# Kernel tuning notes

Measured on AMD Instinct MI355X. Metric: run time of the kernel, lower is better.

## Reference

```python
import jax, jax.numpy as jnp
import numpy as np

B, H_HIST, S_DIM, HID, G, K, A = 1024, 16384, 32, 64, 10, 4, 8


def setup_inputs() -> dict:
    key = jax.random.key(0)
    ks = jax.random.split(key, 12)
    inp = {
        'state_batch': jax.random.normal(ks[0], (B, S_DIM), jnp.float32),
        'state_history_batch': jax.random.normal(ks[1], (H_HIST, S_DIM), jnp.float32),
        'joint_action_history_batch': jax.random.normal(ks[2], (H_HIST, G, A), jnp.float32),
        # per-abstract-agent encoder MLP: Linear(S->H) + ReLU, Linear(H->H) + ReLU, Linear(H->H) + ReLU
        'W0': jax.random.normal(ks[3], (K, S_DIM, HID), jnp.float32) / np.sqrt(S_DIM),
        'b0': jax.random.normal(ks[4], (K, HID), jnp.float32) * 0.01,
        'W1': jax.random.normal(ks[5], (K, HID, HID), jnp.float32) / np.sqrt(HID),
        'b1': jax.random.normal(ks[6], (K, HID), jnp.float32) * 0.01,
        'W2': jax.random.normal(ks[7], (K, HID, HID), jnp.float32) / np.sqrt(HID),
        'b2': jax.random.normal(ks[8], (K, HID), jnp.float32) * 0.01,
        'assignment_matrix': jnp.ones((G, K), jnp.float32),
    }
    return inp


def _encode(x, W0, b0, W1, b1, W2, b2):
    # x: [N, S_DIM] shared across K encoders -> [K, N, HID]
    h = jax.nn.relu(jnp.einsum('ni,kio->kno', x, W0) + b0[:, None, :])
    h = jax.nn.relu(jnp.einsum('kni,kio->kno', h, W1) + b1[:, None, :])
    h = jax.nn.relu(jnp.einsum('kni,kio->kno', h, W2) + b2[:, None, :])
    return h


def reference(state_batch, state_history_batch, joint_action_history_batch,
              W0, b0, W1, b1, W2, b2, assignment_matrix):
    enc_s = _encode(state_batch, W0, b0, W1, b1, W2, b2)            # [K, B, HID]
    enc_h = _encode(state_history_batch, W0, b0, W1, b1, W2, b2)    # [K, H, HID]
    # per (abstract agent k, batch item b): softmax over history of <enc_h, enc_s>
    attn = jax.nn.softmax(jnp.einsum('khd,kbd->kbh', enc_h, enc_s), axis=-1)  # [K, B, H]
    # weighted action aggregation: [H,G,A] contracted over H
    abs_pred = jnp.einsum('kbh,hga->kbga', attn, joint_action_history_batch)  # [K, B, G, A]
    soft_assign = jax.nn.softmax(assignment_matrix, axis=-1)                  # [G, K]
    out = jnp.einsum('gk,kbga->bga', soft_assign, abs_pred)                   # [B, G, A]
    return out
```

## Files before the change

kernel.cpp:

```cpp
#include <hip/hip_runtime.h>
#include <stdint.h>

#define B_SZ 1024
#define H_SZ 16384
#define SD   32
#define HID  64
#define G_SZ 10
#define K_SZ 4
#define A_SZ 8
#define VA   80

typedef float f32x4  __attribute__((ext_vector_type(4)));
typedef short bf16x8 __attribute__((ext_vector_type(8)));

__device__ inline short f2bf(float a) {
    unsigned u = __float_as_uint(a);
    return (short)((u + 0x7FFFu + ((u >> 16) & 1u)) >> 16);
}
__device__ inline void split_bf(float v, short& hi, short& lo) {
    hi = f2bf(v);
    lo = f2bf(v - __uint_as_float(((unsigned)(unsigned short)hi) << 16));
}
__device__ inline int cvt_pk_bf16(float a, float b) {
    int r;
    asm("v_cvt_pk_bf16_f32 %0, %1, %2" : "=v"(r) : "v"(a), "v"(b));
    return r;
}
__device__ inline void split2(float f0, float f1, int& hi, int& lo) {
    hi = cvt_pk_bf16(f0, f1);
    float r0 = f0 - __uint_as_float((unsigned)hi << 16);
    float r1 = f1 - __uint_as_float((unsigned)hi & 0xFFFF0000u);
    lo = cvt_pk_bf16(r0, r1);
}

__global__ __launch_bounds__(256) void k_prep(
    const float* __restrict__ W0, const float* __restrict__ W1,
    const float* __restrict__ W2,
    short* __restrict__ w0h, short* __restrict__ w0l,
    short* __restrict__ w1h, short* __restrict__ w1l,
    short* __restrict__ w2h, short* __restrict__ w2l)
{
    int idx = blockIdx.x * 256 + threadIdx.x;
    short hh, ll;
    if (idx < 8192) {
        int k = idx >> 11, r = idx & 2047;
        int i = r >> 6, jj = r & 63;
        int tt = jj >> 4, l15 = jj & 15;
        int quad = (i >> 3) & 3, e = i & 7;
        split_bf(W0[k * 2048 + i * 64 + jj], hh, ll);
        int dst = k * 2048 + tt * 512 + (quad * 16 + l15) * 8 + e;
        w0h[dst] = hh; w0l[dst] = ll;
    } else if (idx < 24576) {
        int d = idx - 8192;
        int k = d >> 12, r = d & 4095;
        int i = r >> 6, jj = r & 63;
        int kb = i >> 5, quad = (i >> 3) & 3, e = i & 7;
        int tt = jj >> 4, l15 = jj & 15;
        split_bf(W1[k * 4096 + i * 64 + jj], hh, ll);
        int dst = k * 4096 + tt * 1024 + kb * 512 + (quad * 16 + l15) * 8 + e;
        w1h[dst] = hh; w1l[dst] = ll;
    } else if (idx < 40960) {
        int d = idx - 24576;
        int k = d >> 12, r = d & 4095;
        int i = r >> 6, jj = r & 63;
        int kb = i >> 5, quad = (i >> 3) & 3, e = i & 7;
        int tt = jj >> 4, l15 = jj & 15;
        split_bf(W2[k * 4096 + i * 64 + jj], hh, ll);
        int dst = k * 4096 + tt * 1024 + kb * 512 + (quad * 16 + l15) * 8 + e;
        w2h[dst] = hh; w2l[dst] = ll;
    }
}

__global__ __launch_bounds__(256, 3) void k_encode(
    const float* __restrict__ state, const float* __restrict__ hist,
    const float* __restrict__ act,
    const short* __restrict__ w0fh, const short* __restrict__ w0fl,
    const short* __restrict__ w1fh, const short* __restrict__ w1fl,
    const short* __restrict__ w2fh, const short* __restrict__ w2fl,
    const float* __restrict__ b0, const float* __restrict__ b1,
    const float* __restrict__ b2,
    short* __restrict__ enc_s_h, short* __restrict__ enc_s_l,
    short* __restrict__ kf_h, short* __restrict__ kf_l,
    short* __restrict__ vf_h, short* __restrict__ vf_l)
{
    __shared__ __align__(16) short smem[18432];
    const int bid = blockIdx.x;
    const int t = threadIdx.x;

    if (bid >= 1088) {
        short* tile_h = smem;
        short* tile_l = smem + 5376;
        const int h0 = (bid - 1088) * 64;
        #pragma unroll
        for (int i = 0; i < 10; ++i) {
            int idx2 = 2 * (t + i * 256);
            float2 v = *(const float2*)(act + (size_t)h0 * VA + idx2);
            int h = idx2 / 80, c = idx2 - h * 80;
            int hi, lo; split2(v.x, v.y, hi, lo);
            *(int*)(tile_h + h * 84 + c) = hi;
            *(int*)(tile_l + h * 84 + c) = lo;
        }
        __syncthreads();
        #pragma unroll
        for (int i = 0; i < 3; ++i) {
            int jj = t + i * 256;
            if (jj < 640) {
                int va = jj >> 3, hb = jj & 7;
                union { short s[8]; uint4 v; } uh, ul;
                #pragma unroll
                for (int uu = 0; uu < 8; ++uu) {
                    uh.s[uu] = tile_h[(hb * 8 + uu) * 84 + va];
                    ul.s[uu] = tile_l[(hb * 8 + uu) * 84 + va];
                }
                int vtile = (h0 >> 5) + (hb >> 2);
                int lanep = ((hb & 3) << 4) | (va & 15);
                size_t a = (size_t)vtile * 2560 + (va >> 4) * 512 + lanep * 8;
                *(uint4*)(vf_h + a) = uh.v;
                *(uint4*)(vf_l + a) = ul.v;
            }
        }
        return;
    }

    const int k = bid / 272;
    const int tl = bid % 272;
    const bool is_state = (tl < 16);
    const float qscale = is_state ? 1.44269504f : 1.0f;
    const float* X = is_state ? state + (size_t)tl * 64 * SD
                              : hist + (size_t)(tl - 16) * 64 * SD;
    short* dst_h = enc_s_h + ((size_t)k * B_SZ + tl * 64) * HID;
    short* dst_l = enc_s_l + ((size_t)k * B_SZ + tl * 64) * HID;

    short* xt_h  = smem;
    short* xt_l  = smem + 2560;
    short* hb2_h = smem;
    short* hb2_l = smem + 4608;
    short* hb1_h = smem + 9216;
    short* hb1_l = smem + 13824;
    short* ot_h  = smem + 9216;
    short* ot_l  = smem + 13824;

    {
        int r = t >> 2, c0 = (t & 3) * 8;
        const float* src = X + r * SD + c0;
        #pragma unroll
        for (int u = 0; u < 4; ++u) {
            float2 v = *(const float2*)(src + 2 * u);
            int hi, lo; split2(v.x, v.y, hi, lo);
            *(int*)(xt_h + r * 40 + c0 + 2 * u) = hi;
            *(int*)(xt_l + r * 40 + c0 + 2 * u) = lo;
        }
    }
    __syncthreads();

    const int w = t >> 6, l15 = t & 15, quad = (t >> 4) & 3, lane = t & 63;
    const f32x4 fz = {0.f, 0.f, 0.f, 0.f};
    const int row0 = w * 16 + quad * 4;

    {
        bf16x8 xa_h = *(const bf16x8*)(xt_h + (w * 16 + l15) * 40 + quad * 8);
        bf16x8 xa_l = *(const bf16x8*)(xt_l + (w * 16 + l15) * 40 + quad * 8);
        const float* b0k = b0 + k * HID;
        const short* wbh = w0fh + k * 2048 + lane * 8;
        const short* wbl = w0fl + k * 2048 + lane * 8;
        #pragma unroll
        for (int tt = 0; tt < 4; ++tt) {
            bf16x8 wf_h = *(const bf16x8*)(wbh + tt * 512);
            bf16x8 wf_l = *(const bf16x8*)(wbl + tt * 512);
            f32x4 c = __builtin_amdgcn_mfma_f32_16x16x32_bf16(xa_h, wf_h, fz, 0, 0, 0);
            c = __builtin_amdgcn_mfma_f32_16x16x32_bf16(xa_l, wf_h, c, 0, 0, 0);
            c = __builtin_amdgcn_mfma_f32_16x16x32_bf16(xa_h, wf_l, c, 0, 0, 0);
            float bias = b0k[l15 + 16 * tt];
            float f0 = fmaxf(c[0] + bias, 0.f), f1 = fmaxf(c[1] + bias, 0.f);
            float f2 = fmaxf(c[2] + bias, 0.f), f3 = fmaxf(c[3] + bias, 0.f);
            int h01, l01, h23, l23;
            split2(f0, f1, h01, l01); split2(f2, f3, h23, l23);
            int cc = l15 + 16 * tt;
            hb1_h[(row0    ) * 72 + cc] = (short)h01;
            hb1_h[(row0 + 1) * 72 + cc] = (short)(h01 >> 16);
            hb1_h[(row0 + 2) * 72 + cc] = (short)h23;
            hb1_h[(row0 + 3) * 72 + cc] = (short)(h23 >> 16);
            hb1_l[(row0    ) * 72 + cc] = (short)l01;
            hb1_l[(row0 + 1) * 72 + cc] = (short)(l01 >> 16);
            hb1_l[(row0 + 2) * 72 + cc] = (short)l23;
            hb1_l[(row0 + 3) * 72 + cc] = (short)(l23 >> 16);
        }
    }
    __syncthreads();
    {
        bf16x8 ha0_h = *(const bf16x8*)(hb1_h + (w * 16 + l15) * 72 + quad * 8);
        bf16x8 ha0_l = *(const bf16x8*)(hb1_l + (w * 16 + l15) * 72 + quad * 8);
        bf16x8 ha1_h = *(const bf16x8*)(hb1_h + (w * 16 + l15) * 72 + 32 + quad * 8);
        bf16x8 ha1_l = *(const bf16x8*)(hb1_l + (w * 16 + l15) * 72 + 32 + quad * 8);
        const float* b1k = b1 + k * HID;
        const short* wbh = w1fh + k * 4096 + lane * 8;
        const short* wbl = w1fl + k * 4096 + lane * 8;
        #pragma unroll
        for (int tt = 0; tt < 4; ++tt) {
            bf16x8 wfa_h = *(const bf16x8*)(wbh + tt * 1024);
            bf16x8 wfb_h = *(const bf16x8*)(wbh + tt * 1024 + 512);
            bf16x8 wfa_l = *(const bf16x8*)(wbl + tt * 1024);
            bf16x8 wfb_l = *(const bf16x8*)(wbl + tt * 1024 + 512);
            f32x4 c = __builtin_amdgcn_mfma_f32_16x16x32_bf16(ha0_h, wfa_h, fz, 0, 0, 0);
            c = __builtin_amdgcn_mfma_f32_16x16x32_bf16(ha1_h, wfb_h, c, 0, 0, 0);
            c = __builtin_amdgcn_mfma_f32_16x16x32_bf16(ha0_l, wfa_h, c, 0, 0, 0);
            c = __builtin_amdgcn_mfma_f32_16x16x32_bf16(ha1_l, wfb_h, c, 0, 0, 0);
            c = __builtin_amdgcn_mfma_f32_16x16x32_bf16(ha0_h, wfa_l, c, 0, 0, 0);
            c = __builtin_amdgcn_mfma_f32_16x16x32_bf16(ha1_h, wfb_l, c, 0, 0, 0);
            float bias = b1k[l15 + 16 * tt];
            float f0 = fmaxf(c[0] + bias, 0.f), f1 = fmaxf(c[1] + bias, 0.f);
            float f2 = fmaxf(c[2] + bias, 0.f), f3 = fmaxf(c[3] + bias, 0.f);
            int h01, l01, h23, l23;
            split2(f0, f1, h01, l01); split2(f2, f3, h23, l23);
            int cc = l15 + 16 * tt;
            hb2_h[(row0    ) * 72 + cc] = (short)h01;
            hb2_h[(row0 + 1) * 72 + cc] = (short)(h01 >> 16);
            hb2_h[(row0 + 2) * 72 + cc] = (short)h23;
            hb2_h[(row0 + 3) * 72 + cc] = (short)(h23 >> 16);
            hb2_l[(row0    ) * 72 + cc] = (short)l01;
            hb2_l[(row0 + 1) * 72 + cc] = (short)(l01 >> 16);
            hb2_l[(row0 + 2) * 72 + cc] = (short)l23;
            hb2_l[(row0 + 3) * 72 + cc] = (short)(l23 >> 16);
        }
    }
    __syncthreads();
    {
        bf16x8 ha0_h = *(const bf16x8*)(hb2_h + (w * 16 + l15) * 72 + quad * 8);
        bf16x8 ha0_l = *(const bf16x8*)(hb2_l + (w * 16 + l15) * 72 + quad * 8);
        bf16x8 ha1_h = *(const bf16x8*)(hb2_h + (w * 16 + l15) * 72 + 32 + quad * 8);
        bf16x8 ha1_l = *(const bf16x8*)(hb2_l + (w * 16 + l15) * 72 + 32 + quad * 8);
        const float* b2k = b2 + k * HID;
        const short* wbh = w2fh + k * 4096 + lane * 8;
        const short* wbl = w2fl + k * 4096 + lane * 8;
        #pragma unroll
        for (int tt = 0; tt < 4; ++tt) {
            bf16x8 wfa_h = *(const bf16x8*)(wbh + tt * 1024);
            bf16x8 wfb_h = *(const bf16x8*)(wbh + tt * 1024 + 512);
            bf16x8 wfa_l = *(const bf16x8*)(wbl + tt * 1024);
            bf16x8 wfb_l = *(const bf16x8*)(wbl + tt * 1024 + 512);
            f32x4 c = __builtin_amdgcn_mfma_f32_16x16x32_bf16(ha0_h, wfa_h, fz, 0, 0, 0);
            c = __builtin_amdgcn_mfma_f32_16x16x32_bf16(ha1_h, wfb_h, c, 0, 0, 0);
            c = __builtin_amdgcn_mfma_f32_16x16x32_bf16(ha0_l, wfa_h, c, 0, 0, 0);
            c = __builtin_amdgcn_mfma_f32_16x16x32_bf16(ha1_l, wfb_h, c, 0, 0, 0);
            c = __builtin_amdgcn_mfma_f32_16x16x32_bf16(ha0_h, wfa_l, c, 0, 0, 0);
            c = __builtin_amdgcn_mfma_f32_16x16x32_bf16(ha1_h, wfb_l, c, 0, 0, 0);
            float bias = b2k[l15 + 16 * tt];
            float f0 = fmaxf(c[0] + bias, 0.f) * qscale;
            float f1 = fmaxf(c[1] + bias, 0.f) * qscale;
            float f2 = fmaxf(c[2] + bias, 0.f) * qscale;
            float f3 = fmaxf(c[3] + bias, 0.f) * qscale;
            int h01, l01, h23, l23;
            split2(f0, f1, h01, l01); split2(f2, f3, h23, l23);
            int cc = l15 + 16 * tt;
            ot_h[(row0    ) * 72 + cc] = (short)h01;
            ot_h[(row0 + 1) * 72 + cc] = (short)(h01 >> 16);
            ot_h[(row0 + 2) * 72 + cc] = (short)h23;
            ot_h[(row0 + 3) * 72 + cc] = (short)(h23 >> 16);
            ot_l[(row0    ) * 72 + cc] = (short)l01;
            ot_l[(row0 + 1) * 72 + cc] = (short)(l01 >> 16);
            ot_l[(row0 + 2) * 72 + cc] = (short)l23;
            ot_l[(row0 + 3) * 72 + cc] = (short)(l23 >> 16);
        }
    }
    __syncthreads();
    if (is_state) {
        #pragma unroll
        for (int u = 0; u < 2; ++u) {
            int id = t * 2 + u;
            int row = id >> 3, c0 = (id & 7) * 8;
            *(uint4*)(dst_h + row * HID + c0) = *(const uint4*)(ot_h + row * 72 + c0);
            *(uint4*)(dst_l + row * HID + c0) = *(const uint4*)(ot_l + row * 72 + c0);
        }
    } else {
        const int ktbase = k * 512 + (tl - 16) * 2;
        #pragma unroll
        for (int u = 0; u < 2; ++u) {
            int id = t * 2 + u;
            int kt2 = id >> 8;
            int f2 = (id >> 6) & 3;
            int lanep = id & 63;
            int hl = kt2 * 32 + ((f2 >> 1) & 1) * 16 + (lanep & 15);
            int c0 = (f2 & 1) * 32 + ((lanep >> 4) & 3) * 8;
            size_t a = (size_t)(ktbase + kt2) * 2048 + f2 * 512 + (size_t)lanep * 8;
            *(uint4*)(kf_h + a) = *(const uint4*)(ot_h + hl * 72 + c0);
            *(uint4*)(kf_l + a) = *(const uint4*)(ot_l + hl * 72 + c0);
        }
    }
}

template<int NCt>
__global__ __launch_bounds__(256, 2) void k_flash(
    const short* __restrict__ enc_s_h, const short* __restrict__ enc_s_l,
    const short* __restrict__ kf_h, const short* __restrict__ kf_l,
    const short* __restrict__ vf_h, const short* __restrict__ vf_l,
    float* __restrict__ Pm, float* __restrict__ Pl, float* __restrict__ Pacc)
{
    constexpr int CHt = H_SZ / NCt;
    constexpr int NT = CHt / 32;
    static_assert(NT % 2 == 0, "NT must be even for 2x unroll");

    const int bid = blockIdx.x;
    const int r8 = bid & 7, j = bid >> 3;
    const int mtile = j & 7, grp = j >> 3;
    const int idx = grp * 8 + r8;
    const int k = idx / NCt, chunk = idx % NCt;
    const int t = threadIdx.x, w = t >> 6, lane = t & 63;
    const int l15 = t & 15, quad = (t >> 4) & 3;
    const int q0 = mtile * 128 + w * 32;
    const f32x4 fz = {0.f, 0.f, 0.f, 0.f};

    bf16x8 qh[2][2], ql[2][2];
    #pragma unroll
    for (int sub = 0; sub < 2; ++sub)
        #pragma unroll
        for (int kb = 0; kb < 2; ++kb) {
            size_t off = ((size_t)k * B_SZ + q0 + sub * 16 + l15) * HID + kb * 32 + quad * 8;
            qh[sub][kb] = *(const bf16x8*)(enc_s_h + off);
            ql[sub][kb] = *(const bf16x8*)(enc_s_l + off);
        }

    f32x4 acc[2][5];
    #pragma unroll
    for (int s = 0; s < 2; ++s)
        #pragma unroll
        for (int tt = 0; tt < 5; ++tt) acc[s][tt] = fz;
    float mrun[2] = {-__builtin_inff(), -__builtin_inff()};
    float lrun[2] = {0.f, 0.f};

    const int tile0 = chunk * NT;
    const short* kbh = kf_h + ((size_t)(k * 512 + tile0)) * 2048 + lane * 8;
    const short* kbl = kf_l + ((size_t)(k * 512 + tile0)) * 2048 + lane * 8;
    const short* vbh = vf_h + (size_t)tile0 * 2560 + lane * 8;
    const short* vbl = vf_l + (size_t)tile0 * 2560 + lane * 8;

    bf16x8 kA[8], kB[8];
    #pragma unroll
    for (int f = 0; f < 4; ++f) {
        kA[f]     = *(const bf16x8*)(kbh + f * 512);
        kA[4 + f] = *(const bf16x8*)(kbl + f * 512);
    }

    auto body = [&](bf16x8 (&kc)[8], bf16x8 (&kn)[8], int it) {
        bf16x8 vh[5], vl[5];
        const short* vph = vbh + (size_t)it * 2560;
        const short* vpl = vbl + (size_t)it * 2560;
        #pragma unroll
        for (int tt = 0; tt < 3; ++tt) {
            vh[tt] = *(const bf16x8*)(vph + tt * 512);
            vl[tt] = *(const bf16x8*)(vpl + tt * 512);
        }
        if (it + 1 < NT) {
            const short* nph = kbh + (size_t)(it + 1) * 2048;
            const short* npl = kbl + (size_t)(it + 1) * 2048;
            #pragma unroll
            for (int f = 0; f < 4; ++f) {
                kn[f]     = *(const bf16x8*)(nph + f * 512);
                kn[4 + f] = *(const bf16x8*)(npl + f * 512);
            }
        }

        f32x4 S[2][2];
        __builtin_amdgcn_s_setprio(1);
        #pragma unroll
        for (int sub = 0; sub < 2; ++sub) {
            f32x4 c = __builtin_amdgcn_mfma_f32_16x16x32_bf16(kc[0], qh[sub][0], fz, 0, 0, 0);
            c = __builtin_amdgcn_mfma_f32_16x16x32_bf16(kc[1], qh[sub][1], c, 0, 0, 0);
            c = __builtin_amdgcn_mfma_f32_16x16x32_bf16(kc[4], qh[sub][0], c, 0, 0, 0);
            c = __builtin_amdgcn_mfma_f32_16x16x32_bf16(kc[5], qh[sub][1], c, 0, 0, 0);
            c = __builtin_amdgcn_mfma_f32_16x16x32_bf16(kc[0], ql[sub][0], c, 0, 0, 0);
            c = __builtin_amdgcn_mfma_f32_16x16x32_bf16(kc[1], ql[sub][1], c, 0, 0, 0);
            S[sub][0] = c;
            f32x4 d = __builtin_amdgcn_mfma_f32_16x16x32_bf16(kc[2], qh[sub][0], fz, 0, 0, 0);
            d = __builtin_amdgcn_mfma_f32_16x16x32_bf16(kc[3], qh[sub][1], d, 0, 0, 0);
            d = __builtin_amdgcn_mfma_f32_16x16x32_bf16(kc[6], qh[sub][0], d, 0, 0, 0);
            d = __builtin_amdgcn_mfma_f32_16x16x32_bf16(kc[7], qh[sub][1], d, 0, 0, 0);
            d = __builtin_amdgcn_mfma_f32_16x16x32_bf16(kc[2], ql[sub][0], d, 0, 0, 0);
            d = __builtin_amdgcn_mfma_f32_16x16x32_bf16(kc[3], ql[sub][1], d, 0, 0, 0);
            S[sub][1] = d;
        }
        __builtin_amdgcn_s_setprio(0);

        #pragma unroll
        for (int tt = 3; tt < 5; ++tt) {
            vh[tt] = *(const bf16x8*)(vph + tt * 512);
            vl[tt] = *(const bf16x8*)(vpl + tt * 512);
        }

        bf16x8 pfv[2];
        #pragma unroll
        for (int sub = 0; sub < 2; ++sub) {
            f32x4 slo = S[sub][0], shi = S[sub][1];
            float a3 = fmaxf(fmaxf(slo[0], slo[1]), slo[2]);
            float b3 = fmaxf(fmaxf(slo[3], shi[0]), shi[1]);
            float c3 = fmaxf(fmaxf(shi[2], shi[3]), a3);
            float tm = fmaxf(b3, c3);
            tm = fmaxf(tm, __shfl_xor(tm, 16));
            tm = fmaxf(tm, __shfl_xor(tm, 32));
            if (__any(tm > mrun[sub])) {
                float mnew = fmaxf(mrun[sub], tm);
                float alpha = exp2f(mrun[sub] - mnew);
                lrun[sub] *= alpha;
                #pragma unroll
                for (int tt = 0; tt < 5; ++tt) acc[sub][tt] = acc[sub][tt] * alpha;
                mrun[sub] = mnew;
            }
            float m = mrun[sub];
            float p0 = exp2f(slo[0] - m), p1 = exp2f(slo[1] - m);
            float p2 = exp2f(slo[2] - m), p3 = exp2f(slo[3] - m);
            float p4 = exp2f(shi[0] - m), p5 = exp2f(shi[1] - m);
            float p6 = exp2f(shi[2] - m), p7 = exp2f(shi[3] - m);
            float ps = (p0 + p1) + (p2 + p3) + (p4 + p5) + (p6 + p7);
            ps += __shfl_xor(ps, 16);
            ps += __shfl_xor(ps, 32);
            lrun[sub] += ps;

            int plo01 = cvt_pk_bf16(p0, p1), plo23 = cvt_pk_bf16(p2, p3);
            int phi01 = cvt_pk_bf16(p4, p5), phi23 = cvt_pk_bf16(p6, p7);
            union { int i[4]; bf16x8 v; } pf;
            #pragma unroll
            for (int jj = 0; jj < 4; ++jj) {
                int src = (((2 * quad + (jj >> 1)) & 3) << 4) + l15;
                int glo = __shfl((jj & 1) ? plo23 : plo01, src);
                int ghi = __shfl((jj & 1) ? phi23 : phi01, src);
                pf.i[jj] = (quad >= 2) ? ghi : glo;
            }
            pfv[sub] = pf.v;
        }

        __builtin_amdgcn_s_setprio(1);
        #pragma unroll
        for (int tt = 0; tt < 5; ++tt) {
            acc[0][tt] = __builtin_amdgcn_mfma_f32_16x16x32_bf16(vh[tt], pfv[0], acc[0][tt], 0, 0, 0);
            acc[0][tt] = __builtin_amdgcn_mfma_f32_16x16x32_bf16(vl[tt], pfv[0], acc[0][tt], 0, 0, 0);
            acc[1][tt] = __builtin_amdgcn_mfma_f32_16x16x32_bf16(vh[tt], pfv[1], acc[1][tt], 0, 0, 0);
            acc[1][tt] = __builtin_amdgcn_mfma_f32_16x16x32_bf16(vl[tt], pfv[1], acc[1][tt], 0, 0, 0);
        }
        __builtin_amdgcn_s_setprio(0);
    };

    for (int ii = 0; ii < NT; ii += 2) {
        body(kA, kB, ii);
        body(kB, kA, ii + 1);
    }

    const int qg = k * B_SZ + q0;
    #pragma unroll
    for (int sub = 0; sub < 2; ++sub) {
        int q = qg + sub * 16 + l15;
        if (quad == 0) {
            Pm[chunk * 4096 + q] = mrun[sub];
            Pl[chunk * 4096 + q] = lrun[sub];
        }
        #pragma unroll
        for (int tt = 0; tt < 5; ++tt)
            #pragma unroll
            for (int r = 0; r < 4; ++r) {
                int va = tt * 16 + quad * 4 + r;
                Pacc[((size_t)chunk * VA + va) * 4096 + q] = acc[sub][tt][r];
            }
    }
}

template<int NCt>
__global__ __launch_bounds__(256) void k_reduce1(
    const float* __restrict__ Pm, const float* __restrict__ Pl,
    const float* __restrict__ Pacc, float* __restrict__ O)
{
    const int bid = blockIdx.x;
    const int qb = bid / 10, vc = bid - qb * 10;
    const int t = threadIdx.x;
    const int q = qb * 64 + (t & 63);
    const int va0 = vc * 8 + (t >> 6) * 2;

    float mc[NCt];
    float M = -__builtin_inff();
    #pragma unroll
    for (int c = 0; c < NCt; ++c) { mc[c] = Pm[c * 4096 + q]; M = fmaxf(M, mc[c]); }
    float L = 0.f;
    float o0 = 0.f, o1 = 0.f;
    #pragma unroll
    for (int c = 0; c < NCt; ++c) {
        float wv = exp2f(mc[c] - M);
        L += wv * Pl[c * 4096 + q];
        o0 += wv * Pacc[((size_t)c * VA + va0) * 4096 + q];
        o1 += wv * Pacc[((size_t)c * VA + va0 + 1) * 4096 + q];
    }
    float inv = 1.f / L;
    O[(size_t)q * VA + va0]     = o0 * inv;
    O[(size_t)q * VA + va0 + 1] = o1 * inv;
}

__global__ __launch_bounds__(256) void k_reduce2(
    const float* __restrict__ O, const float* __restrict__ assign,
    float* __restrict__ out)
{
    const int idx = blockIdx.x * 256 + threadIdx.x;
    const int b = idx / VA, va = idx - b * VA, g = va >> 3;
    const float L2E = 1.44269504f;
    float a0 = assign[g * K_SZ + 0], a1 = assign[g * K_SZ + 1];
    float a2 = assign[g * K_SZ + 2], a3 = assign[g * K_SZ + 3];
    float mx = fmaxf(fmaxf(a0, a1), fmaxf(a2, a3));
    float e0 = exp2f((a0 - mx) * L2E), e1 = exp2f((a1 - mx) * L2E);
    float e2 = exp2f((a2 - mx) * L2E), e3 = exp2f((a3 - mx) * L2E);
    float inv = 1.f / (e0 + e1 + e2 + e3);
    float o = e0 * O[((size_t)(0 * B_SZ + b)) * VA + va]
            + e1 * O[((size_t)(1 * B_SZ + b)) * VA + va]
            + e2 * O[((size_t)(2 * B_SZ + b)) * VA + va]
            + e3 * O[((size_t)(3 * B_SZ + b)) * VA + va];
    out[idx] = o * inv;
}

extern "C" void kernel_launch(void* const* d_in, const int* in_sizes, int n_in,
                              void* d_out, int out_size, void* d_ws, size_t ws_size,
                              hipStream_t stream)
{
    const float* state  = (const float*)d_in[0];
    const float* hist   = (const float*)d_in[1];
    const float* act    = (const float*)d_in[2];
    const float* W0     = (const float*)d_in[3];
    const float* b0     = (const float*)d_in[4];
    const float* W1     = (const float*)d_in[5];
    const float* b1     = (const float*)d_in[6];
    const float* W2     = (const float*)d_in[7];
    const float* b2     = (const float*)d_in[8];
    const float* assign = (const float*)d_in[9];
    float* out = (float*)d_out;

    char* ws = (char*)d_ws;
    short* enc_s_h = (short*)(ws);
    short* enc_s_l = (short*)(ws + 524288);
    short* kf_h    = (short*)(ws + 1048576);
    short* kf_l    = (short*)(ws + 9437184);
    short* vf_h    = (short*)(ws + 17825792);
    short* vf_l    = (short*)(ws + 20447232);
    const size_t base = 23068672;

    const size_t need32 = base + 32ull * (32768 + 1310720) + 1310720 + 163840;
    const int nc = (ws_size >= need32) ? 32 : 16;

    float* Pm   = (float*)(ws + base);
    float* Pl   = (float*)(ws + base + (size_t)nc * 16384);
    float* Pacc = (float*)(ws + base + (size_t)nc * 32768);
    float* O    = (float*)(ws + base + (size_t)nc * 32768 + (size_t)nc * 1310720);
    char*  wt   = (char*)O + 1310720;
    short* w0fh = (short*)(wt);
    short* w0fl = (short*)(wt + 16384);
    short* w1fh = (short*)(wt + 32768);
    short* w1fl = (short*)(wt + 65536);
    short* w2fh = (short*)(wt + 98304);
    short* w2fl = (short*)(wt + 131072);

    k_prep<<<160, 256, 0, stream>>>(W0, W1, W2, w0fh, w0fl, w1fh, w1fl, w2fh, w2fl);
    k_encode<<<1344, 256, 0, stream>>>(state, hist, act,
                                       w0fh, w0fl, w1fh, w1fl, w2fh, w2fl,
                                       b0, b1, b2,
                                       enc_s_h, enc_s_l, kf_h, kf_l, vf_h, vf_l);
    if (nc == 32) {
        k_flash<32><<<1024, 256, 0, stream>>>(enc_s_h, enc_s_l, kf_h, kf_l,
                                              vf_h, vf_l, Pm, Pl, Pacc);
        k_reduce1<32><<<640, 256, 0, stream>>>(Pm, Pl, Pacc, O);
    } else {
        k_flash<16><<<512, 256, 0, stream>>>(enc_s_h, enc_s_l, kf_h, kf_l,
                                             vf_h, vf_l, Pm, Pl, Pacc);
        k_reduce1<16><<<640, 256, 0, stream>>>(Pm, Pl, Pacc, O);
    }
    k_reduce2<<<320, 256, 0, stream>>>(O, assign, out);
}
```

Measured before the change: 164.2 us.

## Fuse split-K reductions with assignment softmax and fix history chunks to sixteen

Merges the two reduction kernels into one that combines the per-chunk flash partials for all four abstract agents and applies the assignment softmax directly, removing the intermediate O buffer and one launch. It also fixes the number of history chunks at 16 instead of picking 32 when workspace allows. Fewer chunks halve the partial traffic and reduction work, but the flash kernel gets 512 blocks instead of 1024, which can lower occupancy in the main attention stage.

```diff
diff --git a/kernel.cpp b/kernel.cpp
--- a/kernel.cpp
+++ b/kernel.cpp
@@ -9,6 +9,7 @@
 #define K_SZ 4
 #define A_SZ 8
 #define VA   80
+#define NC   16
 
 typedef float f32x4  __attribute__((ext_vector_type(4)));
 typedef short bf16x8 __attribute__((ext_vector_type(8)));
@@ -461,53 +462,55 @@
     }
 }
 
-template<int NCt>
-__global__ __launch_bounds__(256) void k_reduce1(
+__global__ __launch_bounds__(256) void k_reduce(
     const float* __restrict__ Pm, const float* __restrict__ Pl,
-    const float* __restrict__ Pacc, float* __restrict__ O)
+    const float* __restrict__ Pacc, const float* __restrict__ assign,
+    float* __restrict__ out)
 {
     const int bid = blockIdx.x;
-    const int qb = bid / 10, vc = bid - qb * 10;
+    const int qb = bid / 20, vcg = bid - qb * 20;
     const int t = threadIdx.x;
-    const int q = qb * 64 + (t & 63);
-    const int va0 = vc * 8 + (t >> 6) * 2;
-
-    float mc[NCt];
-    float M = -__builtin_inff();
-    #pragma unroll
-    for (int c = 0; c < NCt; ++c) { mc[c] = Pm[c * 4096 + q]; M = fmaxf(M, mc[c]); }
-    float L = 0.f;
-    float o0 = 0.f, o1 = 0.f;
-    #pragma unroll
-    for (int c = 0; c < NCt; ++c) {
-        float wv = exp2f(mc[c] - M);
-        L += wv * Pl[c * 4096 + q];
-        o0 += wv * Pacc[((size_t)c * VA + va0) * 4096 + q];
-        o1 += wv * Pacc[((size_t)c * VA + va0 + 1) * 4096 + q];
-    }
-    float inv = 1.f / L;
-    O[(size_t)q * VA + va0]     = o0 * inv;
-    O[(size_t)q * VA + va0 + 1] = o1 * inv;
-}
-
-__global__ __launch_bounds__(256) void k_reduce2(
-    const float* __restrict__ O, const float* __restrict__ assign,
-    float* __restrict__ out)
-{
-    const int idx = blockIdx.x * 256 + threadIdx.x;
-    const int b = idx / VA, va = idx - b * VA, g = va >> 3;
-    const float L2E = 1.44269504f;
+    const int b = qb * 64 + (t & 63);
+    const int va = vcg * 4 + (t >> 6);
+    const int g = va >> 3;
+
+    float mc[K_SZ][NC];
+    float M[K_SZ] = {-__builtin_inff(), -__builtin_inff(),
+                     -__builtin_inff(), -__builtin_inff()};
+    #pragma unroll
+    for (int c = 0; c < NC; ++c)
+        #pragma unroll
+        for (int k = 0; k < K_SZ; ++k) {
+            float m = Pm[c * 4096 + k * B_SZ + b];
+            mc[k][c] = m;
+            M[k] = fmaxf(M[k], m);
+        }
+    float L[K_SZ] = {0.f, 0.f, 0.f, 0.f};
+    #pragma unroll
+    for (int c = 0; c < NC; ++c)
+        #pragma unroll
+        for (int k = 0; k < K_SZ; ++k) {
+            float wv = exp2f(mc[k][c] - M[k]);
+            mc[k][c] = wv;
+            L[k] += wv * Pl[c * 4096 + k * B_SZ + b];
+        }
+    float o[K_SZ] = {0.f, 0.f, 0.f, 0.f};
+    #pragma unroll
+    for (int c = 0; c < NC; ++c)
+        #pragma unroll
+        for (int k = 0; k < K_SZ; ++k)
+            o[k] += mc[k][c] * Pacc[((size_t)(c * VA + va)) * 4096 + k * B_SZ + b];
+
     float a0 = assign[g * K_SZ + 0], a1 = assign[g * K_SZ + 1];
     float a2 = assign[g * K_SZ + 2], a3 = assign[g * K_SZ + 3];
     float mx = fmaxf(fmaxf(a0, a1), fmaxf(a2, a3));
+    const float L2E = 1.44269504f;
     float e0 = exp2f((a0 - mx) * L2E), e1 = exp2f((a1 - mx) * L2E);
     float e2 = exp2f((a2 - mx) * L2E), e3 = exp2f((a3 - mx) * L2E);
     float inv = 1.f / (e0 + e1 + e2 + e3);
-    float o = e0 * O[((size_t)(0 * B_SZ + b)) * VA + va]
-            + e1 * O[((size_t)(1 * B_SZ + b)) * VA + va]
-            + e2 * O[((size_t)(2 * B_SZ + b)) * VA + va]
-            + e3 * O[((size_t)(3 * B_SZ + b)) * VA + va];
-    out[idx] = o * inv;
+    float r = e0 * inv * (o[0] / L[0]) + e1 * inv * (o[1] / L[1])
+            + e2 * inv * (o[2] / L[2]) + e3 * inv * (o[3] / L[3]);
+    out[(size_t)b * VA + va] = r;
 }
 
 extern "C" void kernel_launch(void* const* d_in, const int* in_sizes, int n_in,
@@ -535,14 +538,10 @@
     short* vf_l    = (short*)(ws + 20447232);
     const size_t base = 23068672;
 
-    const size_t need32 = base + 32ull * (32768 + 1310720) + 1310720 + 163840;
-    const int nc = (ws_size >= need32) ? 32 : 16;
-
     float* Pm   = (float*)(ws + base);
-    float* Pl   = (float*)(ws + base + (size_t)nc * 16384);
-    float* Pacc = (float*)(ws + base + (size_t)nc * 32768);
-    float* O    = (float*)(ws + base + (size_t)nc * 32768 + (size_t)nc * 1310720);
-    char*  wt   = (char*)O + 1310720;
+    float* Pl   = (float*)(ws + base + 262144);
+    float* Pacc = (float*)(ws + base + 524288);
+    char*  wt   = ws + base + 524288 + 20971520;
     short* w0fh = (short*)(wt);
     short* w0fl = (short*)(wt + 16384);
     short* w1fh = (short*)(wt + 32768);
@@ -555,14 +554,7 @@
                                        w0fh, w0fl, w1fh, w1fl, w2fh, w2fl,
                                        b0, b1, b2,
                                        enc_s_h, enc_s_l, kf_h, kf_l, vf_h, vf_l);
-    if (nc == 32) {
-        k_flash<32><<<1024, 256, 0, stream>>>(enc_s_h, enc_s_l, kf_h, kf_l,
-                                              vf_h, vf_l, Pm, Pl, Pacc);
-        k_reduce1<32><<<640, 256, 0, stream>>>(Pm, Pl, Pacc, O);
-    } else {
-        k_flash<16><<<512, 256, 0, stream>>>(enc_s_h, enc_s_l, kf_h, kf_l,
-                                             vf_h, vf_l, Pm, Pl, Pacc);
-        k_reduce1<16><<<640, 256, 0, stream>>>(Pm, Pl, Pacc, O);
-    }
-    k_reduce2<<<320, 256, 0, stream>>>(O, assign, out);
-}
+    k_flash<NC><<<512, 256, 0, stream>>>(enc_s_h, enc_s_l, kf_h, kf_l,
+                                         vf_h, vf_l, Pm, Pl, Pacc);
+    k_reduce<<<320, 256, 0, stream>>>(Pm, Pl, Pacc, assign, out);
+}
```

Result: faster. 155.1 us (-5.6%).
